# Kernel optimization log

Measured on AMD Instinct MI355X. Metric: run time of the kernel, lower is better.

## Reference

```python
import jax, jax.numpy as jnp
import numpy as np

G, N, H, L = 128, 32, 128, 6  # graphs, nodes/graph, hidden, conv layers


def _ln(x, g, b, eps=1e-5):
    m = jnp.mean(x, axis=-1, keepdims=True)
    v = jnp.var(x, axis=-1, keepdims=True)
    return (x - m) * jax.lax.rsqrt(v + eps) * g + b


def setup_inputs() -> dict:
    key = jax.random.key(0)
    ks = jax.random.split(key, 16)
    s = float(H) ** -0.5
    return {
        "x_idx": jax.random.randint(ks[0], (G * N,), 0, 32, dtype=jnp.int32),
        "ea_idx": jax.random.randint(ks[1], (G, N, N), 0, 16, dtype=jnp.int32),
        "tf_idx": jax.random.randint(ks[2], (G, N, N), 0, 16, dtype=jnp.int32),
        "adj": jax.random.randint(ks[3], (G, N, N), 0, 2, dtype=jnp.int32),
        "emb_x": 0.2 * jax.random.normal(ks[4], (32, H), dtype=jnp.float32),
        "emb_ea": 0.2 * jax.random.normal(ks[5], (16, H), dtype=jnp.float32),
        "emb_tf": 0.2 * jax.random.normal(ks[6], (16, H), dtype=jnp.float32),
        "W0": s * jax.random.normal(ks[7], (H, H), dtype=jnp.float32),
        "b0": jnp.zeros((H,), jnp.float32),
        "W1": s * jax.random.normal(ks[8], (H, H), dtype=jnp.float32),
        "b1": jnp.zeros((H,), jnp.float32),
        "Wc": s * jax.random.normal(ks[9], (L, H, H), dtype=jnp.float32),
        "bc": jnp.zeros((L, H), jnp.float32),
        "gc": jnp.ones((L, H), jnp.float32),
        "cc": jnp.zeros((L, H), jnp.float32),
        "Wp": s * jax.random.normal(ks[10], (H, H), dtype=jnp.float32),
        "bp": jnp.zeros((H,), jnp.float32),
        "gp": jnp.ones((H,), jnp.float32),
        "cp": jnp.zeros((H,), jnp.float32),
        "Wq1": s * jax.random.normal(ks[11], (H, H), dtype=jnp.float32),
        "bq1": jnp.zeros((H,), jnp.float32),
        "gq1": jnp.ones((H,), jnp.float32),
        "cq1": jnp.zeros((H,), jnp.float32),
        "Wq2": s * jax.random.normal(ks[12], (H, 1), dtype=jnp.float32),
        "bq2": jnp.zeros((1,), jnp.float32),
    }


def reference(x_idx, ea_idx, tf_idx, adj, emb_x, emb_ea, emb_tf,
              W0, b0, W1, b1, Wc, bc, gc, cc, Wp, bp, gp, cp,
              Wq1, bq1, gq1, cq1, Wq2, bq2):
    # InputEncoderSp: embedding lookups
    x = emb_x[x_idx]                                           # [G*N, H]
    Aval = emb_ea[ea_idx] * adj[..., None].astype(emb_ea.dtype)  # [G,N,N,H] masked edge emb
    # tupleinit: unpooling_fromdense1dim gathers lin(x) to tuple dims 0/1
    x0 = (x @ W0 + b0).reshape(G, N, H)
    x1 = (x @ W1 + b1).reshape(G, N, H)
    X = x0[:, :, None, :] * x1[:, None, :, :] * emb_tf[tf_idx]  # [G,N,N,H]
    for l in range(L):
        tX = jax.nn.relu(_ln(X @ Wc[l] + bc[l], gc[l], cc[l]))
        msg = jnp.einsum('gikh,gkjh->gijh', tX, Aval)          # sum_k tX[i,k]*A[k,j]
        X = X + msg
    # OpPoolingSubg2D('S','mean'): pool tuple dim 1 -> node features
    xs = jnp.mean(X, axis=2).reshape(G * N, H)                 # [G*N, H]
    xs = jax.nn.relu(_ln(xs @ Wp + bp, gp, cp))                # poolmlp
    hg = jnp.sum(xs.reshape(G, N, H), axis=1)                  # node->graph sum pool [G,H]
    # pred_lin: 2-layer MLP, tailact=False
    h = jax.nn.relu(_ln(hg @ Wq1 + bq1, gq1, cq1))
    return h @ Wq2 + bq2                                       # [G, num_tasks=1]
```

## Files before the change

kernel.cpp:

```cpp
#include <hip/hip_runtime.h>

#define G 128
#define N 32
#define H 128
#define L 6

typedef _Float16 half8 __attribute__((ext_vector_type(8)));
typedef float f32x4 __attribute__((ext_vector_type(4)));
typedef float f32x16 __attribute__((ext_vector_type(16)));

__global__ __launch_bounds__(256) void k_packW(
    const float* __restrict__ Wc, _Float16* __restrict__ Wpk) {
  int l = blockIdx.x, tid = threadIdx.x;
  const float* W = Wc + (size_t)l * 16384;
  _Float16* hi = Wpk + (size_t)l * 32768;
  _Float16* lo = hi + 16384;
  for (int idx = tid; idx < 16384; idx += 256) {
    int k = idx >> 7, h = idx & 127;
    float v = W[idx];
    _Float16 a = (_Float16)v;
    hi[h * 128 + k] = a;
    lo[h * 128 + k] = (_Float16)(v - (float)a);
  }
}

__global__ __launch_bounds__(256) void k_codes(
    const int* __restrict__ ea_idx, const int* __restrict__ adj,
    unsigned char* __restrict__ codes) {
  int g = blockIdx.x, tid = threadIdx.x;
  int4 ev = ((const int4*)(ea_idx + (size_t)g * 1024))[tid];
  int4 av = ((const int4*)(adj   + (size_t)g * 1024))[tid];
  uchar4 c;
  c.x = av.x ? (unsigned char)ev.x : (unsigned char)16;
  c.y = av.y ? (unsigned char)ev.y : (unsigned char)16;
  c.z = av.z ? (unsigned char)ev.z : (unsigned char)16;
  c.w = av.w ? (unsigned char)ev.w : (unsigned char)16;
  ((uchar4*)(codes + (size_t)g * 1024))[tid] = c;
}

__global__ __launch_bounds__(256) void k_emb_mm(
    const float* __restrict__ emb_x,
    const float* __restrict__ W0, const float* __restrict__ b0, float* __restrict__ P0,
    const float* __restrict__ W1, const float* __restrict__ b1, float* __restrict__ P1) {
  const float* W = blockIdx.x ? W1 : W0;
  const float* b = blockIdx.x ? b1 : b0;
  float*       P = blockIdx.x ? P1 : P0;
  __shared__ float embs_t[128 * 32];
  int tid = threadIdx.x;
  {
    int i = tid & 31, k0 = (tid >> 5) * 16;
    const float* src = emb_x + i * 128 + k0;
#pragma unroll
    for (int m = 0; m < 16; m++) embs_t[(k0 + m) * 32 + i] = src[m];
  }
  __syncthreads();
  int i  = tid >> 3;
  int h0 = (tid & 7) * 16;
  float acc[16];
#pragma unroll
  for (int hh = 0; hh < 16; hh++) acc[hh] = b[h0 + hh];
  for (int k = 0; k < 128; k++) {
    float a = embs_t[k * 32 + i];
    const float4* wr = (const float4*)(W + k * 128 + h0);
    float4 w0 = wr[0], w1 = wr[1], w2 = wr[2], w3 = wr[3];
    acc[0]  += a * w0.x; acc[1]  += a * w0.y; acc[2]  += a * w0.z; acc[3]  += a * w0.w;
    acc[4]  += a * w1.x; acc[5]  += a * w1.y; acc[6]  += a * w1.z; acc[7]  += a * w1.w;
    acc[8]  += a * w2.x; acc[9]  += a * w2.y; acc[10] += a * w2.z; acc[11] += a * w2.w;
    acc[12] += a * w3.x; acc[13] += a * w3.y; acc[14] += a * w3.z; acc[15] += a * w3.w;
  }
  float4* dst = (float4*)(P + i * 128 + h0);
  dst[0] = make_float4(acc[0], acc[1], acc[2], acc[3]);
  dst[1] = make_float4(acc[4], acc[5], acc[6], acc[7]);
  dst[2] = make_float4(acc[8], acc[9], acc[10], acc[11]);
  dst[3] = make_float4(acc[12], acc[13], acc[14], acc[15]);
}

__global__ __launch_bounds__(256) void k_buildX(
    const int* __restrict__ x_idx, const int* __restrict__ tf_idx,
    const float* __restrict__ P0, const float* __restrict__ P1,
    const float* __restrict__ emb_tf, float* __restrict__ Xp) {
  int g = blockIdx.x >> 2, hb = (blockIdx.x & 3) * 32;
  int tid = threadIdx.x;
  __shared__ float x0t[32 * 32];
  __shared__ float x1t[32 * 32];
  __shared__ float etf[32 * 16];
  __shared__ int   tfs[1024];
  {
    int i = tid & 31, h0 = (tid >> 5) * 4;
    int r = x_idx[g * 32 + i];
    const float* s0 = P0 + r * 128 + hb + h0;
    const float* s1 = P1 + r * 128 + hb + h0;
#pragma unroll
    for (int m = 0; m < 4; m++) {
      x0t[(h0 + m) * 32 + i] = s0[m];
      x1t[(h0 + m) * 32 + i] = s1[m];
    }
  }
  if (tid < 32 * 16 / 2) {
    int t = tid & 15, h0 = (tid >> 4) * 2;
    const float* s = emb_tf + t * 128 + hb + h0;
    etf[(h0 + 0) * 16 + t] = s[0];
    etf[(h0 + 1) * 16 + t] = s[1];
  }
  ((int4*)tfs)[tid] = ((const int4*)(tf_idx + (size_t)g * 1024))[tid];
  __syncthreads();
  int i = tid >> 3, j0 = (tid & 7) * 4;
  int t0 = tfs[i * 32 + j0 + 0], t1 = tfs[i * 32 + j0 + 1];
  int t2 = tfs[i * 32 + j0 + 2], t3 = tfs[i * 32 + j0 + 3];
  float* outg = Xp + ((size_t)g << 17) + (size_t)hb * 1024;
  for (int h = 0; h < 32; h++) {
    float a = x0t[h * 32 + i];
    const float* x1r = x1t + h * 32;
    const float* er  = etf + h * 16;
    float4 v;
    v.x = a * x1r[j0 + 0] * er[t0];
    v.y = a * x1r[j0 + 1] * er[t1];
    v.z = a * x1r[j0 + 2] * er[t2];
    v.w = a * x1r[j0 + 3] * er[t3];
    *(float4*)(outg + h * 1024 + tid * 4) = v;
  }
}

__global__ __launch_bounds__(256, 4) void k_conv_mlp(
    const float* __restrict__ Xp, const _Float16* __restrict__ Wpk,
    const float* __restrict__ bcl, const float* __restrict__ gcl,
    const float* __restrict__ ccl, _Float16* __restrict__ tXh) {
  int g = blockIdx.x >> 3, qb = blockIdx.x & 7;
  int tid = threadIdx.x;
  int lane = tid & 63, wv = tid >> 6;
  int x = lane & 15, quad = lane >> 4;
  __shared__ __align__(16) float Xs[32 * 132];

  f32x4 acc[2][8];
#pragma unroll
  for (int hh = 0; hh < 8; hh++) {
    float4 b4 = *(const float4*)(bcl + hh * 16 + quad * 4);
    f32x4 bi; bi[0] = b4.x; bi[1] = b4.y; bi[2] = b4.z; bi[3] = b4.w;
    acc[0][hh] = bi; acc[1][hh] = bi;
  }

  const float* Xg = Xp + ((size_t)g << 17) + qb * 128;
  const _Float16* Wlo = Wpk + 16384;
  int srow = tid >> 3, scol = (tid & 7) * 16;

#pragma unroll 1
  for (int c = 0; c < 4; c++) {
    float4 st[4];
    const float* src = Xg + (size_t)(c * 32 + srow) * 1024 + scol;
#pragma unroll
    for (int m = 0; m < 4; m++) st[m] = ((const float4*)src)[m];
    __syncthreads();
#pragma unroll
    for (int m = 0; m < 4; m++) *(float4*)&Xs[srow * 132 + scol + 4 * m] = st[m];
    __syncthreads();
    half8 bh[2], bl[2];
#pragma unroll
    for (int pt = 0; pt < 2; pt++) {
      int p = wv * 32 + pt * 16 + x;
#pragma unroll
      for (int i = 0; i < 8; i++) {
        float v = Xs[(quad * 8 + i) * 132 + p];
        _Float16 hi = (_Float16)v;
        bh[pt][i] = hi;
        bl[pt][i] = (_Float16)(v - (float)hi);
      }
    }
    int kb = c * 32 + quad * 8;
#pragma unroll
    for (int hh = 0; hh < 8; hh++) {
      int wo = (hh * 16 + x) * 128 + kb;
      half8 ah = *(const half8*)(Wpk + wo);
      half8 al = *(const half8*)(Wlo + wo);
#pragma unroll
      for (int pt = 0; pt < 2; pt++) {
        acc[pt][hh] = __builtin_amdgcn_mfma_f32_16x16x32_f16(ah, bh[pt], acc[pt][hh], 0, 0, 0);
        acc[pt][hh] = __builtin_amdgcn_mfma_f32_16x16x32_f16(ah, bl[pt], acc[pt][hh], 0, 0, 0);
        acc[pt][hh] = __builtin_amdgcn_mfma_f32_16x16x32_f16(al, bh[pt], acc[pt][hh], 0, 0, 0);
      }
    }
  }

  float gm[2], gr[2];
#pragma unroll
  for (int pt = 0; pt < 2; pt++) {
    float s = 0.f;
#pragma unroll
    for (int hh = 0; hh < 8; hh++)
#pragma unroll
      for (int r = 0; r < 4; r++) s += acc[pt][hh][r];
    s += __shfl_xor(s, 16);
    s += __shfl_xor(s, 32);
    float m = s * (1.f / 128.f);
    float qv = 0.f;
#pragma unroll
    for (int hh = 0; hh < 8; hh++)
#pragma unroll
      for (int r = 0; r < 4; r++) { float d = acc[pt][hh][r] - m; qv += d * d; }
    qv += __shfl_xor(qv, 16);
    qv += __shfl_xor(qv, 32);
    gm[pt] = m;
    gr[pt] = rsqrtf(qv * (1.f / 128.f) + 1e-5f);
  }
  int pbase = qb * 128 + wv * 32;
#pragma unroll
  for (int hh = 0; hh < 8; hh++) {
    float4 g4 = *(const float4*)(gcl + hh * 16 + quad * 4);
    float4 c4 = *(const float4*)(ccl + hh * 16 + quad * 4);
    float ga[4] = {g4.x, g4.y, g4.z, g4.w};
    float ca[4] = {c4.x, c4.y, c4.z, c4.w};
#pragma unroll
    for (int r = 0; r < 4; r++) {
      int h = hh * 16 + quad * 4 + r;
      _Float16* dst = tXh + (((size_t)(g * 128 + h)) << 10) + pbase + x;
#pragma unroll
      for (int pt = 0; pt < 2; pt++) {
        float v = (acc[pt][hh][r] - gm[pt]) * gr[pt] * ga[r] + ca[r];
        dst[pt * 16] = (_Float16)fmaxf(v, 0.f);
      }
    }
  }
}

template <bool LAST>
__global__ __launch_bounds__(256) void k_conv_msg(
    const _Float16* __restrict__ tXh, const unsigned char* __restrict__ codes,
    const float* __restrict__ emb_ea,
    float* __restrict__ Xp, float* __restrict__ xs) {
  int g   = blockIdx.x >> 5;
  int hb4 = (blockIdx.x & 31) * 4;
  int tid = threadIdx.x, wv = tid >> 6, lane = tid & 63;
  __shared__ unsigned char c8[1024];
  __shared__ _Float16 ehi[4][20];
  __shared__ _Float16 elo[4][20];
  ((uchar4*)c8)[tid] = ((const uchar4*)(codes + (size_t)g * 1024))[tid];
  if (tid < 64) {
    int hh = tid >> 4, e = tid & 15;
    float v = emb_ea[e * 128 + hb4 + hh];
    _Float16 hi = (_Float16)v;
    ehi[hh][e] = hi;
    elo[hh][e] = (_Float16)(v - (float)hi);
  } else if (tid < 68) {
    ehi[tid - 64][16] = (_Float16)0.f;
    elo[tid - 64][16] = (_Float16)0.f;
  }
  __syncthreads();

  int h = hb4 + wv;
  int col = lane & 31, khalf = lane >> 5;
  const _Float16* tp = tXh + (((size_t)(g * 128 + h)) << 10) + col * 32 + khalf * 8;
  half8 a0 = *(const half8*)tp;
  half8 a1 = *(const half8*)(tp + 16);
  half8 bh0, bl0, bh1, bl1;
  int kb = khalf * 8;
#pragma unroll
  for (int j = 0; j < 8; j++) {
    int c0 = c8[(kb + j) * 32 + col];
    int c1 = c8[(16 + kb + j) * 32 + col];
    bh0[j] = ehi[wv][c0]; bl0[j] = elo[wv][c0];
    bh1[j] = ehi[wv][c1]; bl1[j] = elo[wv][c1];
  }
  f32x16 acc = {};
  acc = __builtin_amdgcn_mfma_f32_32x32x16_f16(a0, bh0, acc, 0, 0, 0);
  acc = __builtin_amdgcn_mfma_f32_32x32x16_f16(a0, bl0, acc, 0, 0, 0);
  acc = __builtin_amdgcn_mfma_f32_32x32x16_f16(a1, bh1, acc, 0, 0, 0);
  acc = __builtin_amdgcn_mfma_f32_32x32x16_f16(a1, bl1, acc, 0, 0, 0);

  float* xr = Xp + (((size_t)(g * 128 + h)) << 10);
  if (!LAST) {
#pragma unroll
    for (int reg = 0; reg < 16; reg++) {
      int row = (reg & 3) + 8 * (reg >> 2) + 4 * khalf;
      float* p = xr + row * 32 + col;
      *p += acc[reg];
    }
  } else {
#pragma unroll
    for (int reg = 0; reg < 16; reg++) {
      int row = (reg & 3) + 8 * (reg >> 2) + 4 * khalf;
      float s = xr[row * 32 + col] + acc[reg];
      s += __shfl_xor(s, 1);  s += __shfl_xor(s, 2);  s += __shfl_xor(s, 4);
      s += __shfl_xor(s, 8);  s += __shfl_xor(s, 16);
      if (col == 0) xs[((size_t)(g * 32 + row)) * 128 + h] = s * (1.f / 32.f);
    }
  }
}

__global__ __launch_bounds__(256) void k_tail2(
    const float* __restrict__ xs,
    const float* __restrict__ Wp, const float* __restrict__ bp,
    const float* __restrict__ gp, const float* __restrict__ cp,
    const float* __restrict__ Wq1, const float* __restrict__ bq1,
    const float* __restrict__ gq1, const float* __restrict__ cq1,
    const float* __restrict__ Wq2, const float* __restrict__ bq2,
    float* __restrict__ out) {
  int g = blockIdx.x, tid = threadIdx.x;
  __shared__ float xsl[32 * 132];
  __shared__ float y_s[32 * 132];
  __shared__ float red8[32][9];
  __shared__ float hg_s[128];
  __shared__ float q_s[128];
  __shared__ float stat[2];
  {
    const float4* src = (const float4*)(xs + (size_t)g * 4096);
#pragma unroll
    for (int m = 0; m < 4; m++) {
      int f = m * 256 + tid;
      int row = f >> 5, col = (f & 31) * 4;
      *(float4*)&xsl[row * 132 + col] = src[f];
    }
  }
  __syncthreads();
  int i_ = tid >> 3, ht = tid & 7, h0 = ht * 16;
  float acc[16];
#pragma unroll
  for (int hh = 0; hh < 16; hh++) acc[hh] = bp[h0 + hh];
  for (int k = 0; k < 128; k++) {
    float a = xsl[i_ * 132 + k];
    const float4* wr = (const float4*)(Wp + k * 128 + h0);
    float4 w0 = wr[0], w1 = wr[1], w2 = wr[2], w3 = wr[3];
    acc[0]  += a * w0.x; acc[1]  += a * w0.y; acc[2]  += a * w0.z; acc[3]  += a * w0.w;
    acc[4]  += a * w1.x; acc[5]  += a * w1.y; acc[6]  += a * w1.z; acc[7]  += a * w1.w;
    acc[8]  += a * w2.x; acc[9]  += a * w2.y; acc[10] += a * w2.z; acc[11] += a * w2.w;
    acc[12] += a * w3.x; acc[13] += a * w3.y; acc[14] += a * w3.z; acc[15] += a * w3.w;
  }
  {
    float s = 0.f;
#pragma unroll
    for (int hh = 0; hh < 16; hh++) s += acc[hh];
    red8[i_][ht] = s;
  }
  __syncthreads();
  float m = 0.f;
#pragma unroll
  for (int t = 0; t < 8; t++) m += red8[i_][t];
  m *= (1.f / 128.f);
  __syncthreads();
  {
    float q = 0.f;
#pragma unroll
    for (int hh = 0; hh < 16; hh++) { float d = acc[hh] - m; q += d * d; }
    red8[i_][ht] = q;
  }
  __syncthreads();
  float v = 0.f;
#pragma unroll
  for (int t = 0; t < 8; t++) v += red8[i_][t];
  float r = rsqrtf(v * (1.f / 128.f) + 1e-5f);
#pragma unroll
  for (int hh = 0; hh < 16; hh++) {
    int hcol = h0 + hh;
    y_s[i_ * 132 + hcol] = fmaxf((acc[hh] - m) * r * gp[hcol] + cp[hcol], 0.f);
  }
  __syncthreads();
  if (tid < 128) {
    float sh = 0.f;
#pragma unroll
    for (int ii = 0; ii < 32; ii++) sh += y_s[ii * 132 + tid];
    hg_s[tid] = sh;
  }
  __syncthreads();
  if (tid < 128) {
    float a = bq1[tid];
    for (int k = 0; k < 128; k++) a += hg_s[k] * Wq1[k * 128 + tid];
    q_s[tid] = a;
  }
  __syncthreads();
  if (tid < 64) {
    float s2 = q_s[tid] + q_s[tid + 64];
    s2 += __shfl_xor(s2, 1);  s2 += __shfl_xor(s2, 2);  s2 += __shfl_xor(s2, 4);
    s2 += __shfl_xor(s2, 8);  s2 += __shfl_xor(s2, 16); s2 += __shfl_xor(s2, 32);
    if (tid == 0) stat[0] = s2 * (1.f / 128.f);
  }
  __syncthreads();
  float mq = stat[0];
  if (tid < 64) {
    float d0 = q_s[tid] - mq, d1 = q_s[tid + 64] - mq;
    float v2 = d0 * d0 + d1 * d1;
    v2 += __shfl_xor(v2, 1);  v2 += __shfl_xor(v2, 2);  v2 += __shfl_xor(v2, 4);
    v2 += __shfl_xor(v2, 8);  v2 += __shfl_xor(v2, 16); v2 += __shfl_xor(v2, 32);
    if (tid == 0) stat[1] = rsqrtf(v2 * (1.f / 128.f) + 1e-5f);
  }
  __syncthreads();
  float rq = stat[1];
  if (tid < 64) {
    float a0 = fmaxf((q_s[tid]      - mq) * rq * gq1[tid]      + cq1[tid],      0.f) * Wq2[tid];
    float a1 = fmaxf((q_s[tid + 64] - mq) * rq * gq1[tid + 64] + cq1[tid + 64], 0.f) * Wq2[tid + 64];
    float t = a0 + a1;
    t += __shfl_xor(t, 1);  t += __shfl_xor(t, 2);  t += __shfl_xor(t, 4);
    t += __shfl_xor(t, 8);  t += __shfl_xor(t, 16); t += __shfl_xor(t, 32);
    if (tid == 0) out[g] = t + bq2[0];
  }
}

extern "C" void kernel_launch(void* const* d_in, const int* in_sizes, int n_in,
                              void* d_out, int out_size, void* d_ws, size_t ws_size,
                              hipStream_t stream) {
  const int*   x_idx  = (const int*)d_in[0];
  const int*   ea_idx = (const int*)d_in[1];
  const int*   tf_idx = (const int*)d_in[2];
  const int*   adj    = (const int*)d_in[3];
  const float* emb_x  = (const float*)d_in[4];
  const float* emb_ea = (const float*)d_in[5];
  const float* emb_tf = (const float*)d_in[6];
  const float* W0  = (const float*)d_in[7];
  const float* b0  = (const float*)d_in[8];
  const float* W1  = (const float*)d_in[9];
  const float* b1  = (const float*)d_in[10];
  const float* Wc  = (const float*)d_in[11];
  const float* bc  = (const float*)d_in[12];
  const float* gc  = (const float*)d_in[13];
  const float* cc  = (const float*)d_in[14];
  const float* Wp  = (const float*)d_in[15];
  const float* bp  = (const float*)d_in[16];
  const float* gp  = (const float*)d_in[17];
  const float* cp  = (const float*)d_in[18];
  const float* Wq1 = (const float*)d_in[19];
  const float* bq1 = (const float*)d_in[20];
  const float* gq1 = (const float*)d_in[21];
  const float* cq1 = (const float*)d_in[22];
  const float* Wq2 = (const float*)d_in[23];
  const float* bq2 = (const float*)d_in[24];
  float* out = (float*)d_out;

  float* ws  = (float*)d_ws;
  float* Xp  = ws;
  _Float16* tXh = (_Float16*)(ws + (size_t)16777216);
  float* P0  = ws + (size_t)33554432;
  float* P1  = P0 + 4096;
  float* xs  = ws + (size_t)33562624;
  _Float16* Wpk = (_Float16*)(ws + (size_t)34086912);
  unsigned char* codes = (unsigned char*)(ws + (size_t)34185216);

  k_packW<<<6, 256, 0, stream>>>(Wc, Wpk);
  k_codes<<<G, 256, 0, stream>>>(ea_idx, adj, codes);
  k_emb_mm<<<2, 256, 0, stream>>>(emb_x, W0, b0, P0, W1, b1, P1);
  k_buildX<<<G * 4, 256, 0, stream>>>(x_idx, tf_idx, P0, P1, emb_tf, Xp);
  for (int l = 0; l < L; l++) {
    k_conv_mlp<<<G * 8, 256, 0, stream>>>(Xp, Wpk + (size_t)l * 32768,
                                          bc + l * H, gc + l * H, cc + l * H, tXh);
    if (l < L - 1)
      k_conv_msg<false><<<G * 32, 256, 0, stream>>>(tXh, codes, emb_ea, Xp, xs);
    else
      k_conv_msg<true><<<G * 32, 256, 0, stream>>>(tXh, codes, emb_ea, Xp, xs);
  }
  k_tail2<<<G, 256, 0, stream>>>(xs, Wp, bp, gp, cp, Wq1, bq1, gq1, cq1, Wq2, bq2, out);
}
```

Baseline: 730.4 us.

## Switch residual X to tuple-major layout and stage msg/tX through shared memory

The persistent fp32 state X moves from feature-major [g][h][i][j] to tuple-major [g][p][h] storage. The MLP kernel can then read its operand rows directly from global memory with contiguous float4 loads, with no LDS transpose and barriers. Its fp16 output goes through a shared tile so it can be written back in coalesced 16-byte chunks. The message kernel now handles 16 features per block, buffers results in LDS and applies the residual with coalesced float4 read-modify-writes. The cost is much more LDS per block (about 32KB in the MLP kernel and about 67KB in the message kernel) and fewer, larger blocks, which lowers occupancy.

```diff
diff --git a/kernel.cpp b/kernel.cpp
--- a/kernel.cpp
+++ b/kernel.cpp
@@ -79,45 +79,57 @@
     const int* __restrict__ x_idx, const int* __restrict__ tf_idx,
     const float* __restrict__ P0, const float* __restrict__ P1,
     const float* __restrict__ emb_tf, float* __restrict__ Xp) {
-  int g = blockIdx.x >> 2, hb = (blockIdx.x & 3) * 32;
-  int tid = threadIdx.x;
-  __shared__ float x0t[32 * 32];
-  __shared__ float x1t[32 * 32];
-  __shared__ float etf[32 * 16];
-  __shared__ int   tfs[1024];
-  {
-    int i = tid & 31, h0 = (tid >> 5) * 4;
+  int g = blockIdx.x, tid = threadIdx.x;
+  __shared__ float x0t[32 * 132];
+  __shared__ float x1t[32 * 132];
+  __shared__ float etf[16 * 132];
+  __shared__ unsigned char tfs[1024];
+  {
+    int i = tid >> 3, hq = (tid & 7) * 16;
     int r = x_idx[g * 32 + i];
-    const float* s0 = P0 + r * 128 + hb + h0;
-    const float* s1 = P1 + r * 128 + hb + h0;
+    const float4* s0 = (const float4*)(P0 + r * 128 + hq);
+    const float4* s1 = (const float4*)(P1 + r * 128 + hq);
 #pragma unroll
     for (int m = 0; m < 4; m++) {
-      x0t[(h0 + m) * 32 + i] = s0[m];
-      x1t[(h0 + m) * 32 + i] = s1[m];
-    }
-  }
-  if (tid < 32 * 16 / 2) {
-    int t = tid & 15, h0 = (tid >> 4) * 2;
-    const float* s = emb_tf + t * 128 + hb + h0;
-    etf[(h0 + 0) * 16 + t] = s[0];
-    etf[(h0 + 1) * 16 + t] = s[1];
-  }
-  ((int4*)tfs)[tid] = ((const int4*)(tf_idx + (size_t)g * 1024))[tid];
-  __syncthreads();
-  int i = tid >> 3, j0 = (tid & 7) * 4;
-  int t0 = tfs[i * 32 + j0 + 0], t1 = tfs[i * 32 + j0 + 1];
-  int t2 = tfs[i * 32 + j0 + 2], t3 = tfs[i * 32 + j0 + 3];
-  float* outg = Xp + ((size_t)g << 17) + (size_t)hb * 1024;
-  for (int h = 0; h < 32; h++) {
-    float a = x0t[h * 32 + i];
-    const float* x1r = x1t + h * 32;
-    const float* er  = etf + h * 16;
-    float4 v;
-    v.x = a * x1r[j0 + 0] * er[t0];
-    v.y = a * x1r[j0 + 1] * er[t1];
-    v.z = a * x1r[j0 + 2] * er[t2];
-    v.w = a * x1r[j0 + 3] * er[t3];
-    *(float4*)(outg + h * 1024 + tid * 4) = v;
+      *(float4*)&x0t[i * 132 + hq + 4 * m] = s0[m];
+      *(float4*)&x1t[i * 132 + hq + 4 * m] = s1[m];
+    }
+  }
+  if (tid < 128) {
+    int t = tid >> 3, hq = (tid & 7) * 16;
+    const float4* s = (const float4*)(emb_tf + t * 128 + hq);
+#pragma unroll
+    for (int m = 0; m < 4; m++) *(float4*)&etf[t * 132 + hq + 4 * m] = s[m];
+  }
+  {
+    int4 tv = ((const int4*)(tf_idx + (size_t)g * 1024))[tid];
+    uchar4 c;
+    c.x = (unsigned char)tv.x; c.y = (unsigned char)tv.y;
+    c.z = (unsigned char)tv.z; c.w = (unsigned char)tv.w;
+    ((uchar4*)tfs)[tid] = c;
+  }
+  __syncthreads();
+  float* outg = Xp + ((size_t)g << 17);
+#pragma unroll 1
+  for (int pp = 0; pp < 4; pp++) {
+    int p = tid + 256 * pp;
+    int i = p >> 5, j = p & 31, t = tfs[p];
+    const float* a = x0t + i * 132;
+    const float* b = x1t + j * 132;
+    const float* e = etf + t * 132;
+    float* dst = outg + (size_t)p * 128;
+#pragma unroll
+    for (int hq = 0; hq < 32; hq++) {
+      float4 av = *(const float4*)(a + hq * 4);
+      float4 bv = *(const float4*)(b + hq * 4);
+      float4 ev = *(const float4*)(e + hq * 4);
+      float4 v;
+      v.x = av.x * bv.x * ev.x;
+      v.y = av.y * bv.y * ev.y;
+      v.z = av.z * bv.z * ev.z;
+      v.w = av.w * bv.w * ev.w;
+      *(float4*)(dst + hq * 4) = v;
+    }
   }
 }
 
@@ -129,7 +141,7 @@
   int tid = threadIdx.x;
   int lane = tid & 63, wv = tid >> 6;
   int x = lane & 15, quad = lane >> 4;
-  __shared__ __align__(16) float Xs[32 * 132];
+  __shared__ _Float16 tXs[128 * 128];
 
   f32x4 acc[2][8];
 #pragma unroll
@@ -139,33 +151,26 @@
     acc[0][hh] = bi; acc[1][hh] = bi;
   }
 
-  const float* Xg = Xp + ((size_t)g << 17) + qb * 128;
+  const float* Xg = Xp + ((size_t)g << 17) + (size_t)(qb * 128) * 128;
   const _Float16* Wlo = Wpk + 16384;
-  int srow = tid >> 3, scol = (tid & 7) * 16;
 
 #pragma unroll 1
   for (int c = 0; c < 4; c++) {
-    float4 st[4];
-    const float* src = Xg + (size_t)(c * 32 + srow) * 1024 + scol;
-#pragma unroll
-    for (int m = 0; m < 4; m++) st[m] = ((const float4*)src)[m];
-    __syncthreads();
-#pragma unroll
-    for (int m = 0; m < 4; m++) *(float4*)&Xs[srow * 132 + scol + 4 * m] = st[m];
-    __syncthreads();
+    int kb = c * 32 + quad * 8;
     half8 bh[2], bl[2];
 #pragma unroll
     for (int pt = 0; pt < 2; pt++) {
-      int p = wv * 32 + pt * 16 + x;
+      const float* xc = Xg + (size_t)(wv * 32 + pt * 16 + x) * 128 + kb;
+      float4 f0 = ((const float4*)xc)[0];
+      float4 f1 = ((const float4*)xc)[1];
+      float vv[8] = {f0.x, f0.y, f0.z, f0.w, f1.x, f1.y, f1.z, f1.w};
 #pragma unroll
       for (int i = 0; i < 8; i++) {
-        float v = Xs[(quad * 8 + i) * 132 + p];
-        _Float16 hi = (_Float16)v;
+        _Float16 hi = (_Float16)vv[i];
         bh[pt][i] = hi;
-        bl[pt][i] = (_Float16)(v - (float)hi);
-      }
-    }
-    int kb = c * 32 + quad * 8;
+        bl[pt][i] = (_Float16)(vv[i] - (float)hi);
+      }
+    }
 #pragma unroll
     for (int hh = 0; hh < 8; hh++) {
       int wo = (hh * 16 + x) * 128 + kb;
@@ -201,7 +206,6 @@
     gm[pt] = m;
     gr[pt] = rsqrtf(qv * (1.f / 128.f) + 1e-5f);
   }
-  int pbase = qb * 128 + wv * 32;
 #pragma unroll
   for (int hh = 0; hh < 8; hh++) {
     float4 g4 = *(const float4*)(gcl + hh * 16 + quad * 4);
@@ -211,76 +215,124 @@
 #pragma unroll
     for (int r = 0; r < 4; r++) {
       int h = hh * 16 + quad * 4 + r;
-      _Float16* dst = tXh + (((size_t)(g * 128 + h)) << 10) + pbase + x;
 #pragma unroll
       for (int pt = 0; pt < 2; pt++) {
         float v = (acc[pt][hh][r] - gm[pt]) * gr[pt] * ga[r] + ca[r];
-        dst[pt * 16] = (_Float16)fmaxf(v, 0.f);
-      }
-    }
+        tXs[h * 128 + wv * 32 + pt * 16 + x] = (_Float16)fmaxf(v, 0.f);
+      }
+    }
+  }
+  __syncthreads();
+  const uint4* src = (const uint4*)tXs;
+  _Float16* outb = tXh + ((size_t)(g * 128)) * 1024 + qb * 128;
+#pragma unroll
+  for (int m = 0; m < 8; m++) {
+    int f = m * 256 + tid;
+    int row = f >> 4, seg = f & 15;
+    *(uint4*)(outb + (size_t)row * 1024 + seg * 8) = src[f];
   }
 }
 
 template <bool LAST>
-__global__ __launch_bounds__(256) void k_conv_msg(
+__global__ __launch_bounds__(256, 2) void k_conv_msg(
     const _Float16* __restrict__ tXh, const unsigned char* __restrict__ codes,
     const float* __restrict__ emb_ea,
     float* __restrict__ Xp, float* __restrict__ xs) {
-  int g   = blockIdx.x >> 5;
-  int hb4 = (blockIdx.x & 31) * 4;
+  int g  = blockIdx.x >> 3;
+  int hb = (blockIdx.x & 7) * 16;
   int tid = threadIdx.x, wv = tid >> 6, lane = tid & 63;
   __shared__ unsigned char c8[1024];
-  __shared__ _Float16 ehi[4][20];
-  __shared__ _Float16 elo[4][20];
+  __shared__ _Float16 ehi[16][20];
+  __shared__ _Float16 elo[16][20];
+  __shared__ float mb[16 * 1056];
   ((uchar4*)c8)[tid] = ((const uchar4*)(codes + (size_t)g * 1024))[tid];
-  if (tid < 64) {
-    int hh = tid >> 4, e = tid & 15;
-    float v = emb_ea[e * 128 + hb4 + hh];
+  {
+    int hl = tid >> 4, e = tid & 15;
+    float v = emb_ea[e * 128 + hb + hl];
     _Float16 hi = (_Float16)v;
-    ehi[hh][e] = hi;
-    elo[hh][e] = (_Float16)(v - (float)hi);
-  } else if (tid < 68) {
-    ehi[tid - 64][16] = (_Float16)0.f;
-    elo[tid - 64][16] = (_Float16)0.f;
-  }
-  __syncthreads();
-
-  int h = hb4 + wv;
+    ehi[hl][e] = hi;
+    elo[hl][e] = (_Float16)(v - (float)hi);
+  }
+  if (tid < 16) { ehi[tid][16] = (_Float16)0.f; elo[tid][16] = (_Float16)0.f; }
+  __syncthreads();
+
   int col = lane & 31, khalf = lane >> 5;
-  const _Float16* tp = tXh + (((size_t)(g * 128 + h)) << 10) + col * 32 + khalf * 8;
-  half8 a0 = *(const half8*)tp;
-  half8 a1 = *(const half8*)(tp + 16);
-  half8 bh0, bl0, bh1, bl1;
-  int kb = khalf * 8;
-#pragma unroll
-  for (int j = 0; j < 8; j++) {
-    int c0 = c8[(kb + j) * 32 + col];
-    int c1 = c8[(16 + kb + j) * 32 + col];
-    bh0[j] = ehi[wv][c0]; bl0[j] = elo[wv][c0];
-    bh1[j] = ehi[wv][c1]; bl1[j] = elo[wv][c1];
-  }
-  f32x16 acc = {};
-  acc = __builtin_amdgcn_mfma_f32_32x32x16_f16(a0, bh0, acc, 0, 0, 0);
-  acc = __builtin_amdgcn_mfma_f32_32x32x16_f16(a0, bl0, acc, 0, 0, 0);
-  acc = __builtin_amdgcn_mfma_f32_32x32x16_f16(a1, bh1, acc, 0, 0, 0);
-  acc = __builtin_amdgcn_mfma_f32_32x32x16_f16(a1, bl1, acc, 0, 0, 0);
-
-  float* xr = Xp + (((size_t)(g * 128 + h)) << 10);
-  if (!LAST) {
+#pragma unroll 1
+  for (int s = 0; s < 4; s++) {
+    int hl = wv * 4 + s, h = hb + hl;
+    const _Float16* tp = tXh + (((size_t)(g * 128 + h)) << 10) + col * 32 + khalf * 8;
+    half8 b0 = *(const half8*)tp;
+    half8 b1 = *(const half8*)(tp + 16);
+    half8 ah0, al0, ah1, al1;
+    int kb = khalf * 8;
+#pragma unroll
+    for (int j = 0; j < 8; j++) {
+      int c0 = c8[(kb + j) * 32 + col];
+      int c1 = c8[(kb + 16 + j) * 32 + col];
+      ah0[j] = ehi[hl][c0]; al0[j] = elo[hl][c0];
+      ah1[j] = ehi[hl][c1]; al1[j] = elo[hl][c1];
+    }
+    f32x16 acc = {};
+    acc = __builtin_amdgcn_mfma_f32_32x32x16_f16(ah0, b0, acc, 0, 0, 0);
+    acc = __builtin_amdgcn_mfma_f32_32x32x16_f16(al0, b0, acc, 0, 0, 0);
+    acc = __builtin_amdgcn_mfma_f32_32x32x16_f16(ah1, b1, acc, 0, 0, 0);
+    acc = __builtin_amdgcn_mfma_f32_32x32x16_f16(al1, b1, acc, 0, 0, 0);
+    float* mrow = mb + hl * 1056;
 #pragma unroll
     for (int reg = 0; reg < 16; reg++) {
       int row = (reg & 3) + 8 * (reg >> 2) + 4 * khalf;
-      float* p = xr + row * 32 + col;
-      *p += acc[reg];
-    }
-  } else {
-#pragma unroll
-    for (int reg = 0; reg < 16; reg++) {
-      int row = (reg & 3) + 8 * (reg >> 2) + 4 * khalf;
-      float s = xr[row * 32 + col] + acc[reg];
-      s += __shfl_xor(s, 1);  s += __shfl_xor(s, 2);  s += __shfl_xor(s, 4);
-      s += __shfl_xor(s, 8);  s += __shfl_xor(s, 16);
-      if (col == 0) xs[((size_t)(g * 32 + row)) * 128 + h] = s * (1.f / 32.f);
+      mrow[row * 33 + col] = acc[reg];
+    }
+  }
+  __syncthreads();
+#pragma unroll 1
+  for (int pp = 0; pp < 4; pp++) {
+    int p = tid + 256 * pp;
+    int i = p >> 5, j = p & 31;
+    float* xr = Xp + ((size_t)g << 17) + (size_t)p * 128 + hb;
+    float4 xv[4];
+#pragma unroll
+    for (int m = 0; m < 4; m++) xv[m] = ((const float4*)xr)[m];
+    const float* mcol = mb + j * 33 + i;
+    float mv[16];
+#pragma unroll
+    for (int hl = 0; hl < 16; hl++) mv[hl] = mcol[hl * 1056];
+#pragma unroll
+    for (int m = 0; m < 4; m++) {
+      xv[m].x += mv[4 * m + 0];
+      xv[m].y += mv[4 * m + 1];
+      xv[m].z += mv[4 * m + 2];
+      xv[m].w += mv[4 * m + 3];
+    }
+    if (!LAST) {
+#pragma unroll
+      for (int m = 0; m < 4; m++) ((float4*)xr)[m] = xv[m];
+    } else {
+      float fv[16];
+#pragma unroll
+      for (int m = 0; m < 4; m++) {
+        fv[4 * m + 0] = xv[m].x; fv[4 * m + 1] = xv[m].y;
+        fv[4 * m + 2] = xv[m].z; fv[4 * m + 3] = xv[m].w;
+      }
+#pragma unroll
+      for (int hl = 0; hl < 16; hl++) {
+        float v = fv[hl];
+        v += __shfl_xor(v, 1);  v += __shfl_xor(v, 2);  v += __shfl_xor(v, 4);
+        v += __shfl_xor(v, 8);  v += __shfl_xor(v, 16);
+        fv[hl] = v;
+      }
+      if (j == 0) {
+        float* xo = xs + ((size_t)(g * 32 + i)) * 128 + hb;
+#pragma unroll
+        for (int m = 0; m < 4; m++) {
+          float4 o;
+          o.x = fv[4 * m + 0] * (1.f / 32.f);
+          o.y = fv[4 * m + 1] * (1.f / 32.f);
+          o.z = fv[4 * m + 2] * (1.f / 32.f);
+          o.w = fv[4 * m + 3] * (1.f / 32.f);
+          ((float4*)xo)[m] = o;
+        }
+      }
     }
   }
 }
@@ -434,14 +486,14 @@
   k_packW<<<6, 256, 0, stream>>>(Wc, Wpk);
   k_codes<<<G, 256, 0, stream>>>(ea_idx, adj, codes);
   k_emb_mm<<<2, 256, 0, stream>>>(emb_x, W0, b0, P0, W1, b1, P1);
-  k_buildX<<<G * 4, 256, 0, stream>>>(x_idx, tf_idx, P0, P1, emb_tf, Xp);
+  k_buildX<<<G, 256, 0, stream>>>(x_idx, tf_idx, P0, P1, emb_tf, Xp);
   for (int l = 0; l < L; l++) {
     k_conv_mlp<<<G * 8, 256, 0, stream>>>(Xp, Wpk + (size_t)l * 32768,
                                           bc + l * H, gc + l * H, cc + l * H, tXh);
     if (l < L - 1)
-      k_conv_msg<false><<<G * 32, 256, 0, stream>>>(tXh, codes, emb_ea, Xp, xs);
+      k_conv_msg<false><<<G * 8, 256, 0, stream>>>(tXh, codes, emb_ea, Xp, xs);
     else
-      k_conv_msg<true><<<G * 32, 256, 0, stream>>>(tXh, codes, emb_ea, Xp, xs);
+      k_conv_msg<true><<<G * 8, 256, 0, stream>>>(tXh, codes, emb_ea, Xp, xs);
   }
   k_tail2<<<G, 256, 0, stream>>>(xs, Wp, bp, gp, cp, Wq1, bq1, gq1, cq1, Wq2, bq2, out);
 }
```

Result: slower. 996.5 us (+36.4%).
